# Performance work log

Hardware: AMD Instinct MI355X
Metric: run time of the kernel (lower is better)

The kernel has to match this reference:

```python
import jax, jax.numpy as jnp
import numpy as np

N, E, G = 50000, 800000, 256
NODE_IN, EDGE_IN, H, L, RO, OUT = 64, 16, 128, 3, 128, 2
EPS = 1e-5


def _ln(x, g, b):
    m = jnp.mean(x, axis=-1, keepdims=True)
    v = jnp.mean((x - m) ** 2, axis=-1, keepdims=True)
    return (x - m) * jax.lax.rsqrt(v + EPS) * g + b


def setup_inputs() -> dict:
    key = jax.random.key(0)
    ks = iter(jax.random.split(key, 40))
    w = lambda *s: jax.random.normal(next(ks), s, dtype=jnp.float32) * 0.05
    inp = {
        "x": jax.random.normal(next(ks), (N, NODE_IN), dtype=jnp.float32),
        "edge_attr": jax.random.normal(next(ks), (E, EDGE_IN), dtype=jnp.float32),
        "edge_index": jax.random.randint(next(ks), (2, E), 0, N, dtype=jnp.int32),
        "batch": jnp.sort(jax.random.randint(next(ks), (N,), 0, G, dtype=jnp.int32)),
        # encoders + input norms
        "node_enc_w": w(NODE_IN, H), "node_enc_b": jnp.zeros((H,), jnp.float32),
        "edge_enc_w": w(EDGE_IN, H), "edge_enc_b": jnp.zeros((H,), jnp.float32),
        "node_ln_g": jnp.ones((H,), jnp.float32), "node_ln_b": jnp.zeros((H,), jnp.float32),
        "edge_ln_g": jnp.ones((H,), jnp.float32), "edge_ln_b": jnp.zeros((H,), jnp.float32),
        # per-layer stacked params [L, ...]
        "msg_w1": w(L, 2 * H, H), "msg_b1": jnp.zeros((L, H), jnp.float32),
        "msg_w2": w(L, H, H), "msg_b2": jnp.zeros((L, H), jnp.float32),
        "gate_w": w(L, 2 * H, H), "gate_b": jnp.zeros((L, H), jnp.float32),
        "res_w1": w(L, 2 * H, H), "res_b1": jnp.zeros((L, H), jnp.float32),
        "res_w2": w(L, H, H), "res_b2": jnp.zeros((L, H), jnp.float32),
        "ln_g": jnp.ones((L, H), jnp.float32), "ln_b": jnp.zeros((L, H), jnp.float32),
        # readout MLP
        "ro_w1": w(H, RO), "ro_b1": jnp.zeros((RO,), jnp.float32),
        "ro_w2": w(RO, OUT), "ro_b2": jnp.zeros((OUT,), jnp.float32),
    }
    return inp


def reference(x, edge_attr, edge_index, batch,
              node_enc_w, node_enc_b, edge_enc_w, edge_enc_b,
              node_ln_g, node_ln_b, edge_ln_g, edge_ln_b,
              msg_w1, msg_b1, msg_w2, msg_b2, gate_w, gate_b,
              res_w1, res_b1, res_w2, res_b2, ln_g, ln_b,
              ro_w1, ro_b1, ro_w2, ro_b2):
    src, dst = edge_index[0], edge_index[1]
    h = _ln(x @ node_enc_w + node_enc_b, node_ln_g, node_ln_b)        # [N,H]
    e = _ln(edge_attr @ edge_enc_w + edge_enc_b, edge_ln_g, edge_ln_b)  # [E,H]
    for l in range(L):
        cat = jnp.concatenate([h[src], e], axis=-1)                   # [E,2H]
        gate = jax.nn.sigmoid(cat @ gate_w[l] + gate_b[l])
        msg = jax.nn.relu(cat @ msg_w1[l] + msg_b1[l]) @ msg_w2[l] + msg_b2[l]
        agg = jax.ops.segment_sum(gate * msg, dst, num_segments=N)    # scatter-add
        comb = jnp.concatenate([h, agg], axis=-1)                     # [N,2H]
        res = jax.nn.relu(comb @ res_w1[l] + res_b1[l]) @ res_w2[l] + res_b2[l]
        h = _ln(h + res, ln_g[l], ln_b[l])
    # global mean pool over graphs
    sums = jax.ops.segment_sum(h, batch, num_segments=G)              # [G,H]
    cnt = jax.ops.segment_sum(jnp.ones((h.shape[0],), h.dtype), batch, num_segments=G)
    g = sums / jnp.maximum(cnt, 1.0)[:, None]
    return jax.nn.relu(g @ ro_w1 + ro_b1) @ ro_w2 + ro_b2             # [G,OUT]
```

## Files before the change

kernel.cpp:

```cpp
#include <hip/hip_runtime.h>
#include <math.h>

#define NN 50000
#define NE 800000
#define NG 256
#define H 128
#define NIN 64
#define EIN 16
#define NL 3
#define LEPS 1e-5f

typedef short bf16x8 __attribute__((ext_vector_type(8)));
typedef float f32x4 __attribute__((ext_vector_type(4)));
typedef float f32x16 __attribute__((ext_vector_type(16)));

__device__ __forceinline__ short bf16rne(float x) {
  unsigned u = __float_as_uint(x);
  unsigned r = u + 0x7fff + ((u >> 16) & 1);
  return (short)(r >> 16);
}

__device__ __forceinline__ float wsum(float v) {
#pragma unroll
  for (int m = 1; m < 64; m <<= 1) v += __shfl_xor(v, m, 64);
  return v;
}

__device__ __forceinline__ float lds_f32(const short* p) {
  short2 s = *(const short2*)p;
  return __uint_as_float((unsigned)(unsigned short)s.x |
                         ((unsigned)(unsigned short)s.y << 16));
}

__global__ __launch_bounds__(256) void k_count(const int* __restrict__ eidx,
                                               unsigned* __restrict__ cnt) {
  int t = blockIdx.x * 256 + threadIdx.x;
  if (t < NE) atomicAdd(&cnt[eidx[NE + t]], 1u);
}

__global__ __launch_bounds__(1024) void k_scan(const unsigned* __restrict__ cnt,
                                               unsigned* __restrict__ rowptr) {
  __shared__ unsigned part[16];
  __shared__ unsigned carry_s;
  const int tid = threadIdx.x, lane = tid & 63, wid = tid >> 6;
  if (tid == 0) carry_s = 0;
  __syncthreads();
  for (int base = 0; base < NN; base += 1024) {
    int i = base + tid;
    unsigned v = (i < NN) ? cnt[i] : 0u;
    unsigned incl = v;
#pragma unroll
    for (int off = 1; off < 64; off <<= 1) {
      unsigned t = __shfl_up(incl, off, 64);
      if (lane >= off) incl += t;
    }
    if (lane == 63) part[wid] = incl;
    __syncthreads();
    if (tid == 0) {
      unsigned s = 0;
#pragma unroll
      for (int w = 0; w < 16; w++) { unsigned t = part[w]; part[w] = s; s += t; }
    }
    __syncthreads();
    unsigned carry = carry_s;
    if (i < NN) rowptr[i] = carry + part[wid] + incl - v;
    __syncthreads();
    if (tid == 1023) carry_s = carry + part[15] + incl;
    __syncthreads();
  }
}

__global__ __launch_bounds__(256) void k_fold(
    const float* __restrict__ gate_w, const float* __restrict__ msg_w1,
    const float* __restrict__ e_enc_w, const float* __restrict__ e_enc_b,
    const float* __restrict__ e_ln_g, const float* __restrict__ e_ln_b,
    short* __restrict__ w2e, float* __restrict__ c123,
    float* __restrict__ stats) {
  const int S_W2E = 3 * 4096;
  const int S_C = S_W2E + 3 * 768;
  const int S_ST = S_C + 290;
  int tid = blockIdx.x * 256 + threadIdx.x;
  if (tid >= S_ST) return;
  if (tid < S_W2E) {
    int l = tid / 4096, e = tid % 4096;
    int t = e >> 9, lane = (e >> 3) & 63, j = e & 7;
    int k = (lane >> 5) * 8 + j;
    int n = t * 32 + (lane & 31);
    float s = 0.f;
    for (int m = 0; m < 128; m++) {
      float w = (n < 128) ? gate_w[((size_t)l * 256 + 128 + m) * 128 + n]
                          : msg_w1[((size_t)l * 256 + 128 + m) * 128 + (n - 128)];
      s += e_enc_w[k * 128 + m] * e_ln_g[m] * w;
    }
    w2e[tid] = bf16rne(s);
  } else if (tid < S_C) {
    int e = tid - S_W2E;
    int l = e / 768, r = e % 768, which = r / 256, n = r % 256;
    float s = 0.f;
    for (int m = 0; m < 128; m++) {
      float w = (n < 128) ? gate_w[((size_t)l * 256 + 128 + m) * 128 + n]
                          : msg_w1[((size_t)l * 256 + 128 + m) * 128 + (n - 128)];
      float f = (which == 0) ? e_enc_b[m] * e_ln_g[m]
              : (which == 1) ? e_ln_g[m] : e_ln_b[m];
      s += f * w;
    }
    c123[e] = s;
  } else {
    int e = tid - S_C;
    if (e < 256) {
      int i = e >> 4, j = e & 15;
      float s = 0.f;
      for (int n = 0; n < 128; n++)
        s += e_enc_w[i * 128 + n] * e_enc_w[j * 128 + n];
      stats[e] = s;
    } else if (e < 272) {
      int k = e - 256;
      float s = 0.f;
      for (int n = 0; n < 128; n++) s += e_enc_w[k * 128 + n];
      stats[e] = s;
    } else if (e < 288) {
      int k = e - 272;
      float s = 0.f;
      for (int n = 0; n < 128; n++) s += e_enc_w[k * 128 + n] * e_enc_b[n];
      stats[e] = s;
    } else if (e == 288) {
      float s = 0.f;
      for (int n = 0; n < 128; n++) s += e_enc_b[n] * e_enc_b[n];
      stats[e] = s;
    } else {
      float s = 0.f;
      for (int n = 0; n < 128; n++) s += e_enc_b[n];
      stats[e] = s;
    }
  }
}

__global__ __launch_bounds__(256) void k_scatter(
    const int* __restrict__ eidx, const float* __restrict__ ea,
    const unsigned* __restrict__ rowptr, unsigned* __restrict__ cursor,
    const float* __restrict__ stats,
    int* __restrict__ src_s, int* __restrict__ dst_s,
    short* __restrict__ ea_bf, float2* __restrict__ rsmu) {
  __shared__ float S[290];
  for (int i = threadIdx.x; i < 290; i += 256) S[i] = stats[i];
  __syncthreads();
  int t = blockIdx.x * 256 + threadIdx.x;
  int s = eidx[t], d = eidx[NE + t];
  unsigned pos = rowptr[d] + atomicAdd(&cursor[d], 1u);
  src_s[pos] = s;
  dst_s[pos] = d;
  const float4* er = (const float4*)(ea + (size_t)t * EIN);
  float4 q0 = er[0], q1 = er[1], q2 = er[2], q3 = er[3];
  float e16[16];
  e16[0]=q0.x; e16[1]=q0.y; e16[2]=q0.z; e16[3]=q0.w;
  e16[4]=q1.x; e16[5]=q1.y; e16[6]=q1.z; e16[7]=q1.w;
  e16[8]=q2.x; e16[9]=q2.y; e16[10]=q2.z; e16[11]=q2.w;
  e16[12]=q3.x; e16[13]=q3.y; e16[14]=q3.z; e16[15]=q3.w;
  short tmp[16];
#pragma unroll
  for (int j = 0; j < 16; j++) tmp[j] = bf16rne(e16[j]);
  short* dstp = ea_bf + (size_t)pos * EIN;
  *(bf16x8*)dstp = *(bf16x8*)tmp;
  *(bf16x8*)(dstp + 8) = *(bf16x8*)(tmp + 8);
  float s1 = S[289], s2 = S[288];
#pragma unroll
  for (int k = 0; k < 16; k++) {
    s1 = fmaf(e16[k], S[256 + k], s1);
    s2 = fmaf(2.f * e16[k], S[272 + k], s2);
  }
#pragma unroll
  for (int i = 0; i < 16; i++) {
    float mi = 0.f;
#pragma unroll
    for (int j = 0; j < 16; j++) mi = fmaf(S[i * 16 + j], e16[j], mi);
    s2 = fmaf(e16[i], mi, s2);
  }
  float mu = s1 * (1.f / 128.f);
  float var = s2 * (1.f / 128.f) - mu * mu;
  float rs = rsqrtf(var + LEPS);
  rsmu[pos] = make_float2(rs, mu);
}

__global__ __launch_bounds__(256) void k_convert_w(
    const float* __restrict__ gate_w, const float* __restrict__ msg_w1,
    const float* __restrict__ msg_w2, const float* __restrict__ e_enc_w,
    const float* __restrict__ res_w1, const float* __restrict__ res_w2,
    short* __restrict__ bgh, short* __restrict__ bm2, short* __restrict__ benc,
    short* __restrict__ brs1, short* __restrict__ brs2) {
  const int S_BGH = 3 * 65536;
  const int S_BM2 = S_BGH + 3 * 16384;
  const int S_BEN = S_BM2 + 2048;
  const int S_BR1 = S_BEN + 3 * 32768;
  const int S_BR2 = S_BR1 + 3 * 16384;
  int tid = blockIdx.x * 256 + threadIdx.x;
  if (tid >= S_BR2) return;
  if (tid < S_BGH) {
    int l = tid / 65536, e = tid % 65536;
    int f = e >> 9, lane = (e >> 3) & 63, j = e & 7;
    int nt = f >> 4, ks = f & 15;
    int k = ks * 16 + (lane >> 5) * 8 + j;
    int n = nt * 32 + (lane & 31);
    float v = (n < 128) ? gate_w[((size_t)l * 256 + k) * 128 + n]
                        : msg_w1[((size_t)l * 256 + k) * 128 + (n - 128)];
    bgh[tid] = bf16rne(v);
  } else if (tid < S_BM2) {
    int e0 = tid - S_BGH;
    int l = e0 / 16384, e = e0 % 16384;
    int f = e >> 9, lane = (e >> 3) & 63, j = e & 7;
    int nt = f >> 3, ks = f & 7;
    int k = ks * 16 + (lane >> 5) * 8 + j;
    int n = nt * 32 + (lane & 31);
    bm2[e0] = bf16rne(msg_w2[((size_t)l * 128 + k) * 128 + n]);
  } else if (tid < S_BEN) {
    int e = tid - S_BM2;
    int t = e >> 9, lane = (e >> 3) & 63, j = e & 7;
    int k = (lane >> 5) * 8 + j;
    int n = t * 32 + (lane & 31);
    benc[e] = bf16rne(e_enc_w[k * H + n]);
  } else if (tid < S_BR1) {
    int e0 = tid - S_BEN;
    int l = e0 / 32768, e = e0 % 32768;
    int f = e >> 9, lane = (e >> 3) & 63, j = e & 7;
    int nt = f >> 3, ks = f & 7;
    int k = ks * 32 + (lane >> 4) * 8 + j;
    int n = nt * 16 + (lane & 15);
    brs1[e0] = bf16rne(res_w1[((size_t)l * 256 + k) * 128 + n]);
  } else {
    int e0 = tid - S_BR1;
    int l = e0 / 16384, e = e0 % 16384;
    int f = e >> 9, lane = (e >> 3) & 63, j = e & 7;
    int nt = f >> 2, ks = f & 3;
    int k = ks * 32 + (lane >> 4) * 8 + j;
    int n = nt * 16 + (lane & 15);
    brs2[e0] = bf16rne(res_w2[((size_t)l * 128 + k) * 128 + n]);
  }
}

__global__ __launch_bounds__(256) void k_node_encode(
    const float* __restrict__ x, const float* __restrict__ W,
    const float* __restrict__ bias,
    const float* __restrict__ lng, const float* __restrict__ lnb,
    float* __restrict__ h, short* __restrict__ h_bf) {
  __shared__ float xs[4][8 * NIN];
  const int wave = threadIdx.x >> 6, lane = threadIdx.x & 63;
  const int n0 = (blockIdx.x * 4 + wave) * 8;
  float* xt = xs[wave];
  for (int i = lane; i < 8 * NIN; i += 64) {
    int idx = n0 * NIN + i;
    xt[i] = (idx < NN * NIN) ? x[idx] : 0.f;
  }
  __syncthreads();
  const int c0 = lane, c1 = lane + 64;
  float a0[8], a1[8];
#pragma unroll
  for (int j = 0; j < 8; j++) { a0[j] = 0.f; a1[j] = 0.f; }
  for (int k = 0; k < NIN; k++) {
    float w0 = W[k * H + c0], w1 = W[k * H + c1];
#pragma unroll
    for (int j = 0; j < 8; j++) {
      float xv = xt[j * NIN + k];
      a0[j] = fmaf(xv, w0, a0[j]);
      a1[j] = fmaf(xv, w1, a1[j]);
    }
  }
  const float b0 = bias[c0], b1 = bias[c1];
  const float g0 = lng[c0], g1 = lng[c1], lb0 = lnb[c0], lb1 = lnb[c1];
#pragma unroll
  for (int j = 0; j < 8; j++) {
    float v0 = a0[j] + b0, v1 = a1[j] + b1;
    float mean = wsum(v0 + v1) * (1.f / H);
    float d0 = v0 - mean, d1 = v1 - mean;
    float var = wsum(d0 * d0 + d1 * d1) * (1.f / H);
    float rs = rsqrtf(var + LEPS);
    int n = n0 + j;
    if (n < NN) {
      float o0 = d0 * rs * g0 + lb0, o1 = d1 * rs * g1 + lb1;
      h[n * H + c0] = o0;
      h[n * H + c1] = o1;
      h_bf[n * H + c0] = bf16rne(o0);
      h_bf[n * H + c1] = bf16rne(o1);
    }
  }
}

__global__ __launch_bounds__(256) void k_edge_mfma(
    const short* __restrict__ ea_bf, const float2* __restrict__ rsmu,
    const int* __restrict__ src_s, const int* __restrict__ dst_s,
    const short* __restrict__ h_bf,
    const short* __restrict__ Bgh, const short* __restrict__ Bm2,
    const short* __restrict__ W2e, const float* __restrict__ c123,
    const float* __restrict__ gbias, const float* __restrict__ mbias1,
    const float* __restrict__ mbias2,
    float* __restrict__ agg) {
  __shared__ short regn[4][32 * 136];
  __shared__ int dsts[4][32];
  __shared__ float rsS[4][32], muS[4][32];
  const int tid = threadIdx.x;
  const int wave = tid >> 6, lane = tid & 63;
  const int e0 = blockIdx.x * 128 + wave * 32;
  short* R = regn[wave];
  const int c31 = lane & 31, halfl = lane >> 5;
  const int koff = halfl * 8;

  if (lane < 32) {
    dsts[wave][lane] = dst_s[e0 + lane];
    float2 rm = rsmu[e0 + lane];
    rsS[wave][lane] = rm.x;
    muS[wave][lane] = rm.y;
  }

  const int srow = src_s[e0 + c31];
  bf16x8 af[8];
#pragma unroll
  for (int ks = 0; ks < 8; ks++)
    af[ks] = *(const bf16x8*)(h_bf + (size_t)srow * H + ks * 16 + koff);

  const float rs_own = rsmu[e0 + c31].x;
  bf16x8 ae;
  {
    bf16x8 raw = *(const bf16x8*)(ea_bf + (size_t)(e0 + c31) * EIN + koff);
#pragma unroll
    for (int j = 0; j < 8; j++) {
      float f = __uint_as_float(((unsigned)(unsigned short)raw[j]) << 16);
      ae[j] = bf16rne(f * rs_own);
    }
  }

  float rsR[16], rmR[16];
#pragma unroll
  for (int r = 0; r < 16; r++) {
    int row = (r & 3) + 8 * (r >> 2) + 4 * halfl;
    rsR[r] = rsS[wave][row];
    rmR[r] = rsR[r] * muS[wave][row];
  }

#pragma unroll
  for (int ht = 0; ht < 4; ht++) {
    const int nt = 4 + ht;
    f32x16 a = __builtin_amdgcn_mfma_f32_32x32x16_bf16(
        ae, *(const bf16x8*)(W2e + (size_t)(nt * 64 + lane) * 8),
        (f32x16)(0.f), 0, 0, 0);
#pragma unroll
    for (int ks = 0; ks < 8; ks++) {
      bf16x8 bf = *(const bf16x8*)(Bgh + (size_t)((nt * 16 + ks) * 64 + lane) * 8);
      a = __builtin_amdgcn_mfma_f32_32x32x16_bf16(af[ks], bf, a, 0, 0, 0);
    }
    const int col = ht * 32 + c31;
    const int n = nt * 32 + c31;
    const float c1v = c123[n], c2v = c123[256 + n];
    const float c3b = c123[512 + n] + mbias1[col];
#pragma unroll
    for (int r = 0; r < 16; r++) {
      int row = (r & 3) + 8 * (r >> 2) + 4 * halfl;
      float pre = fmaf(rsR[r], c1v, fmaf(-rmR[r], c2v, a[r] + c3b));
      R[row * 136 + col] = bf16rne(fmaxf(pre, 0.f));
    }
  }

  float gate[4][16];
#pragma unroll
  for (int gt = 0; gt < 4; gt++) {
    f32x16 a = __builtin_amdgcn_mfma_f32_32x32x16_bf16(
        ae, *(const bf16x8*)(W2e + (size_t)(gt * 64 + lane) * 8),
        (f32x16)(0.f), 0, 0, 0);
#pragma unroll
    for (int ks = 0; ks < 8; ks++) {
      bf16x8 bf = *(const bf16x8*)(Bgh + (size_t)((gt * 16 + ks) * 64 + lane) * 8);
      a = __builtin_amdgcn_mfma_f32_32x32x16_bf16(af[ks], bf, a, 0, 0, 0);
    }
    const int n = gt * 32 + c31;
    const float c1v = c123[n], c2v = c123[256 + n];
    const float c3b = c123[512 + n] + gbias[n];
#pragma unroll
    for (int r = 0; r < 16; r++) {
      float pre = fmaf(rsR[r], c1v, fmaf(-rmR[r], c2v, a[r] + c3b));
      gate[gt][r] = __builtin_amdgcn_rcpf(1.f + __expf(-pre));
    }
  }

  bf16x8 a2[8];
#pragma unroll
  for (int ks = 0; ks < 8; ks++)
    a2[ks] = *(const bf16x8*)&R[c31 * 136 + ks * 16 + koff];

#pragma unroll
  for (int halfM = 0; halfM < 2; halfM++) {
#pragma unroll
    for (int t2 = 0; t2 < 2; t2++) {
      int gt = halfM * 2 + t2;
      f32x16 m = (f32x16)(0.f);
#pragma unroll
      for (int ks = 0; ks < 8; ks++) {
        bf16x8 bf = *(const bf16x8*)(Bm2 + (size_t)((gt * 8 + ks) * 64 + lane) * 8);
        m = __builtin_amdgcn_mfma_f32_32x32x16_bf16(a2[ks], bf, m, 0, 0, 0);
      }
      float mb2 = mbias2[gt * 32 + c31];
      int c2 = t2 * 32 + c31;
#pragma unroll
      for (int r = 0; r < 16; r++) {
        int row = (r & 3) + 8 * (r >> 2) + 4 * halfl;
        float msg = gate[gt][r] * (m[r] + mb2);
        unsigned u = __float_as_uint(msg);
        *(short2*)&R[row * 136 + c2 * 2] =
            make_short2((short)(u & 0xffff), (short)(u >> 16));
      }
    }
    const int colg = halfM * 64 + lane;
    int cur = dsts[wave][0];
    float run = lds_f32(&R[lane * 2]);
#pragma unroll
    for (int row = 1; row < 32; row++) {
      int d = dsts[wave][row];
      float v = lds_f32(&R[row * 136 + lane * 2]);
      if (d == cur) {
        run += v;
      } else {
        atomicAdd(&agg[(size_t)cur * H + colg], run);
        cur = d; run = v;
      }
    }
    atomicAdd(&agg[(size_t)cur * H + colg], run);
  }
}

__global__ __launch_bounds__(256) void k_node_up2(
    float* agg, const short* __restrict__ h_bf_in,
    const float* __restrict__ h_in,
    const short* __restrict__ Brs1, const short* __restrict__ Brs2,
    const float* __restrict__ rb1, const float* __restrict__ rb2,
    const float* __restrict__ lng, const float* __restrict__ lnb,
    float* __restrict__ h, short* __restrict__ h_bf) {
  __shared__ short regn[4][16 * 136];
  const int tid = threadIdx.x;
  const int wave = tid >> 6, lane = tid & 63;
  const int n0 = blockIdx.x * 64 + wave * 16;
  short* R = regn[wave];
  const int mrow = lane & 15, quad = lane >> 4;

  int nr = n0 + mrow; if (nr >= NN) nr = NN - 1;
  bf16x8 af[8];
#pragma unroll
  for (int ks = 0; ks < 4; ks++)
    af[ks] = *(const bf16x8*)(h_bf_in + (size_t)nr * H + ks * 32 + quad * 8);
#pragma unroll
  for (int ks = 0; ks < 4; ks++) {
    float4 u = *(const float4*)(agg + (size_t)nr * H + ks * 32 + quad * 8);
    float4 w = *(const float4*)(agg + (size_t)nr * H + ks * 32 + quad * 8 + 4);
    short tmp[8];
    tmp[0]=bf16rne(u.x); tmp[1]=bf16rne(u.y); tmp[2]=bf16rne(u.z); tmp[3]=bf16rne(u.w);
    tmp[4]=bf16rne(w.x); tmp[5]=bf16rne(w.y); tmp[6]=bf16rne(w.z); tmp[7]=bf16rne(w.w);
    af[4 + ks] = *(bf16x8*)tmp;
  }
  float4 z4 = make_float4(0.f, 0.f, 0.f, 0.f);
#pragma unroll
  for (int ks = 0; ks < 4; ks++) {
    *(float4*)(agg + (size_t)nr * H + ks * 32 + quad * 8) = z4;
    *(float4*)(agg + (size_t)nr * H + ks * 32 + quad * 8 + 4) = z4;
  }

#pragma unroll
  for (int t = 0; t < 8; t++) {
    f32x4 a = (f32x4){0.f, 0.f, 0.f, 0.f};
#pragma unroll
    for (int ks = 0; ks < 8; ks++) {
      bf16x8 bf = *(const bf16x8*)(Brs1 + (size_t)((t * 8 + ks) * 64 + lane) * 8);
      a = __builtin_amdgcn_mfma_f32_16x16x32_bf16(af[ks], bf, a, 0, 0, 0);
    }
    int col = t * 16 + mrow;
    float b = rb1[col];
#pragma unroll
    for (int r = 0; r < 4; r++)
      R[(quad * 4 + r) * 136 + col] = bf16rne(fmaxf(a[r] + b, 0.f));
  }
  bf16x8 a2[4];
#pragma unroll
  for (int ks = 0; ks < 4; ks++)
    a2[ks] = *(const bf16x8*)&R[mrow * 136 + ks * 32 + quad * 8];

  float vals[8][4];
  float gl[8], bl[8];
#pragma unroll
  for (int t = 0; t < 8; t++) {
    f32x4 a = (f32x4){0.f, 0.f, 0.f, 0.f};
#pragma unroll
    for (int ks = 0; ks < 4; ks++) {
      bf16x8 bf = *(const bf16x8*)(Brs2 + (size_t)((t * 4 + ks) * 64 + lane) * 8);
      a = __builtin_amdgcn_mfma_f32_16x16x32_bf16(a2[ks], bf, a, 0, 0, 0);
    }
    int col = t * 16 + mrow;
    float b2 = rb2[col];
    gl[t] = lng[col]; bl[t] = lnb[col];
#pragma unroll
    for (int r = 0; r < 4; r++) {
      int rowi = n0 + quad * 4 + r;
      int rl = rowi < NN ? rowi : NN - 1;
      vals[t][r] = h_in[(size_t)rl * H + col] + a[r] + b2;
    }
  }
#pragma unroll
  for (int r = 0; r < 4; r++) {
    float s1 = 0.f, s2 = 0.f;
#pragma unroll
    for (int t = 0; t < 8; t++) {
      s1 += vals[t][r];
      s2 = fmaf(vals[t][r], vals[t][r], s2);
    }
#pragma unroll
    for (int m = 1; m < 16; m <<= 1) {
      s1 += __shfl_xor(s1, m, 64);
      s2 += __shfl_xor(s2, m, 64);
    }
    float mean = s1 * (1.f / 128.f);
    float var = s2 * (1.f / 128.f) - mean * mean;
    float rs = rsqrtf(var + LEPS);
    int rowi = n0 + quad * 4 + r;
    if (rowi < NN) {
#pragma unroll
      for (int t = 0; t < 8; t++) {
        int col = t * 16 + mrow;
        float o = (vals[t][r] - mean) * rs * gl[t] + bl[t];
        h[(size_t)rowi * H + col] = o;
        h_bf[(size_t)rowi * H + col] = bf16rne(o);
      }
    }
  }
}

__global__ __launch_bounds__(256) void k_pool(
    const float* __restrict__ h, const int* __restrict__ batch,
    float* __restrict__ gsum, float* __restrict__ gcnt) {
  const int tid = threadIdx.x;
  const int col = tid & 127, half = tid >> 7;
  int n0 = blockIdx.x * 32 + half * 16;
  if (n0 >= NN) return;
  int end = n0 + 16; if (end > NN) end = NN;
  int cur = batch[n0];
  float run = h[(size_t)n0 * H + col];
  float cnt = 1.f;
  for (int n = n0 + 1; n < end; n++) {
    int b = batch[n];
    float v = h[(size_t)n * H + col];
    if (b == cur) { run += v; cnt += 1.f; }
    else {
      atomicAdd(&gsum[(size_t)cur * H + col], run);
      if (col == 0) atomicAdd(&gcnt[cur], cnt);
      cur = b; run = v; cnt = 1.f;
    }
  }
  atomicAdd(&gsum[(size_t)cur * H + col], run);
  if (col == 0) atomicAdd(&gcnt[cur], cnt);
}

__global__ __launch_bounds__(128) void k_readout(
    const float* __restrict__ gsum, const float* __restrict__ gcnt,
    const float* __restrict__ W1, const float* __restrict__ b1,
    const float* __restrict__ W2, const float* __restrict__ b2,
    float* __restrict__ out) {
  __shared__ float gs[H];
  __shared__ float o1[H];
  int b = blockIdx.x, c = threadIdx.x;
  float cnt = fmaxf(gcnt[b], 1.f);
  gs[c] = gsum[b * H + c] / cnt;
  __syncthreads();
  float acc = b1[c];
  for (int k = 0; k < H; k++) acc = fmaf(gs[k], W1[k * H + c], acc);
  o1[c] = fmaxf(acc, 0.f);
  __syncthreads();
  if (c < 2) {
    float acc2 = b2[c];
    for (int k = 0; k < H; k++) acc2 = fmaf(o1[k], W2[k * 2 + c], acc2);
    out[b * 2 + c] = acc2;
  }
}

extern "C" void kernel_launch(void* const* d_in, const int* in_sizes, int n_in,
                              void* d_out, int out_size, void* d_ws, size_t ws_size,
                              hipStream_t stream) {
  (void)in_sizes; (void)n_in; (void)out_size; (void)ws_size;
  const float* x       = (const float*)d_in[0];
  const float* ea      = (const float*)d_in[1];
  const int*   eidx    = (const int*)d_in[2];
  const int*   batch   = (const int*)d_in[3];
  const float* n_enc_w = (const float*)d_in[4];
  const float* n_enc_b = (const float*)d_in[5];
  const float* e_enc_w = (const float*)d_in[6];
  const float* e_enc_b = (const float*)d_in[7];
  const float* n_ln_g  = (const float*)d_in[8];
  const float* n_ln_b  = (const float*)d_in[9];
  const float* e_ln_g  = (const float*)d_in[10];
  const float* e_ln_b  = (const float*)d_in[11];
  const float* msg_w1  = (const float*)d_in[12];
  const float* msg_b1  = (const float*)d_in[13];
  const float* msg_w2  = (const float*)d_in[14];
  const float* msg_b2  = (const float*)d_in[15];
  const float* gate_w  = (const float*)d_in[16];
  const float* gate_b  = (const float*)d_in[17];
  const float* res_w1  = (const float*)d_in[18];
  const float* res_b1  = (const float*)d_in[19];
  const float* res_w2  = (const float*)d_in[20];
  const float* res_b2  = (const float*)d_in[21];
  const float* ln_g    = (const float*)d_in[22];
  const float* ln_b    = (const float*)d_in[23];
  const float* ro_w1   = (const float*)d_in[24];
  const float* ro_b1   = (const float*)d_in[25];
  const float* ro_w2   = (const float*)d_in[26];
  const float* ro_b2   = (const float*)d_in[27];

  char* p = (char*)d_ws;
  float* h     = (float*)p;  p += (size_t)NN * H * 4;
  short* h_bf  = (short*)p;  p += (size_t)NN * H * 2;
  float* agg   = (float*)p;  p += (size_t)NN * H * 4;
  short* ea_bf = (short*)p;  p += (size_t)NE * EIN * 2;
  float2* rsmu = (float2*)p; p += (size_t)NE * 8;
  float* gsum  = (float*)p;  p += (size_t)NG * H * 4;
  float* gcnt  = (float*)p;  p += 1024;
  short* bgh   = (short*)p;  p += (size_t)3 * 65536 * 2;
  short* bm2   = (short*)p;  p += (size_t)3 * 16384 * 2;
  short* benc  = (short*)p;  p += (size_t)2048 * 2;
  short* brs1  = (short*)p;  p += (size_t)3 * 32768 * 2;
  short* brs2  = (short*)p;  p += (size_t)3 * 16384 * 2;
  short* w2e   = (short*)p;  p += (size_t)3 * 4096 * 2;
  float* c123  = (float*)p;  p += (size_t)3 * 768 * 4;
  float* stats = (float*)p;  p += 2048;
  unsigned* rowptr = (unsigned*)p; p += ((size_t)NN * 4 + 15) / 16 * 16;
  unsigned* cursor = (unsigned*)p; p += ((size_t)NN * 4 + 15) / 16 * 16;
  int* src_s   = (int*)p;    p += (size_t)NE * 4;
  int* dst_s   = (int*)p;    p += (size_t)NE * 4;

  const int node_blocks = (NN + 31) / 32;
  const int nup_blocks  = (NN + 63) / 64;
  const int edge_blocks = NE / 128;
  const int e256 = (NE + 255) / 256;
  const int conv_total = 3 * 65536 + 3 * 16384 + 2048 + 3 * 32768 + 3 * 16384;
  const int fold_total = 3 * 4096 + 3 * 768 + 290;

  hipMemsetAsync(cursor, 0, (size_t)NN * 4, stream);
  k_fold<<<(fold_total + 255) / 256, 256, 0, stream>>>(
      gate_w, msg_w1, e_enc_w, e_enc_b, e_ln_g, e_ln_b, w2e, c123, stats);
  k_count<<<e256, 256, 0, stream>>>(eidx, cursor);
  k_scan<<<1, 1024, 0, stream>>>(cursor, rowptr);
  hipMemsetAsync(cursor, 0, (size_t)NN * 4, stream);
  k_scatter<<<e256, 256, 0, stream>>>(eidx, ea, rowptr, cursor, stats,
                                      src_s, dst_s, ea_bf, rsmu);

  k_convert_w<<<(conv_total + 255) / 256, 256, 0, stream>>>(
      gate_w, msg_w1, msg_w2, e_enc_w, res_w1, res_w2,
      bgh, bm2, benc, brs1, brs2);
  k_node_encode<<<node_blocks, 256, 0, stream>>>(x, n_enc_w, n_enc_b, n_ln_g, n_ln_b, h, h_bf);

  hipMemsetAsync(agg, 0, (size_t)NN * H * 4, stream);
  for (int l = 0; l < NL; l++) {
    k_edge_mfma<<<edge_blocks, 256, 0, stream>>>(
        ea_bf, rsmu, src_s, dst_s, h_bf,
        bgh + (size_t)l * 65536, bm2 + (size_t)l * 16384,
        w2e + (size_t)l * 4096, c123 + (size_t)l * 768,
        gate_b + l * H, msg_b1 + l * H, msg_b2 + l * H, agg);
    k_node_up2<<<nup_blocks, 256, 0, stream>>>(
        agg, h_bf, h,
        brs1 + (size_t)l * 32768, brs2 + (size_t)l * 16384,
        res_b1 + l * H, res_b2 + l * H,
        ln_g + l * H, ln_b + l * H, h, h_bf);
  }

  hipMemsetAsync(gsum, 0, ((size_t)NG * H + NG) * 4, stream);
  k_pool<<<(NN + 31) / 32, 256, 0, stream>>>(h, batch, gsum, gcnt);
  k_readout<<<NG, 128, 0, stream>>>(gsum, gcnt, ro_w1, ro_b1, ro_w2, ro_b2, (float*)d_out);
}
```

Measured before the change: 1.023 ms.

## Process 64 edges per wave and fold LN correction terms into extra MFMA K-slice

Each wave now handles two 32-edge M-tiles, so every B-fragment loaded from global or L2 feeds two MFMAs, halving weight-fragment traffic per edge. The per-column rs/mu/bias corrections that were applied as scalar FMAs are folded into an extra K=16 slice of the edge weight (rs, -rs*mu, 1 columns), so the MFMA applies them. Gate is recomputed per output tile instead of being kept as a 64-float array, and launch_bounds(256,2) with doubled LDS is set. This raises register and LDS pressure and routes the correction terms through bf16 rounding, which can cost accuracy.

```diff
diff --git a/kernel.cpp b/kernel.cpp
--- a/kernel.cpp
+++ b/kernel.cpp
@@ -1,4 +1,5 @@
 #include <hip/hip_runtime.h>
+#include <hip/hip_bf16.h>
 #include <math.h>
 
 #define NN 50000
@@ -13,11 +14,17 @@
 typedef short bf16x8 __attribute__((ext_vector_type(8)));
 typedef float f32x4 __attribute__((ext_vector_type(4)));
 typedef float f32x16 __attribute__((ext_vector_type(16)));
+typedef unsigned u32x4 __attribute__((ext_vector_type(4)));
 
 __device__ __forceinline__ short bf16rne(float x) {
   unsigned u = __float_as_uint(x);
   unsigned r = u + 0x7fff + ((u >> 16) & 1);
   return (short)(r >> 16);
+}
+
+__device__ __forceinline__ unsigned pk2(float lo, float hi) {
+  __hip_bfloat162 h = __float22bfloat162_rn(make_float2(lo, hi));
+  return *(unsigned*)&h;
 }
 
 __device__ __forceinline__ float wsum(float v) {
@@ -72,41 +79,37 @@
 
 __global__ __launch_bounds__(256) void k_fold(
     const float* __restrict__ gate_w, const float* __restrict__ msg_w1,
+    const float* __restrict__ gate_b, const float* __restrict__ msg_b1,
     const float* __restrict__ e_enc_w, const float* __restrict__ e_enc_b,
     const float* __restrict__ e_ln_g, const float* __restrict__ e_ln_b,
-    short* __restrict__ w2e, float* __restrict__ c123,
-    float* __restrict__ stats) {
-  const int S_W2E = 3 * 4096;
-  const int S_C = S_W2E + 3 * 768;
-  const int S_ST = S_C + 290;
+    short* __restrict__ w2e, float* __restrict__ stats) {
+  const int S_W2E = 3 * 8192;
+  const int S_ST = S_W2E + 290;
   int tid = blockIdx.x * 256 + threadIdx.x;
   if (tid >= S_ST) return;
   if (tid < S_W2E) {
-    int l = tid / 4096, e = tid % 4096;
-    int t = e >> 9, lane = (e >> 3) & 63, j = e & 7;
-    int k = (lane >> 5) * 8 + j;
-    int n = t * 32 + (lane & 31);
+    int l = tid / 8192, e = tid % 8192;
+    int f = e >> 9, lane = (e >> 3) & 63, j = e & 7;
+    int nt = f >> 1, ks2 = f & 1;
+    int k = ks2 * 16 + (lane >> 5) * 8 + j;
+    int n = nt * 32 + (lane & 31);
     float s = 0.f;
-    for (int m = 0; m < 128; m++) {
-      float w = (n < 128) ? gate_w[((size_t)l * 256 + 128 + m) * 128 + n]
-                          : msg_w1[((size_t)l * 256 + 128 + m) * 128 + (n - 128)];
-      s += e_enc_w[k * 128 + m] * e_ln_g[m] * w;
+    if (k < 19) {
+      for (int m = 0; m < 128; m++) {
+        float w = (n < 128) ? gate_w[((size_t)l * 256 + 128 + m) * 128 + n]
+                            : msg_w1[((size_t)l * 256 + 128 + m) * 128 + (n - 128)];
+        float fm = (k < 16)   ? e_enc_w[k * 128 + m] * e_ln_g[m]
+                 : (k == 16)  ? e_enc_b[m] * e_ln_g[m]
+                 : (k == 17)  ? e_ln_g[m]
+                              : e_ln_b[m];
+        s += fm * w;
+      }
+      if (k == 18)
+        s += (n < 128) ? gate_b[l * 128 + n] : msg_b1[l * 128 + (n - 128)];
     }
     w2e[tid] = bf16rne(s);
-  } else if (tid < S_C) {
+  } else {
     int e = tid - S_W2E;
-    int l = e / 768, r = e % 768, which = r / 256, n = r % 256;
-    float s = 0.f;
-    for (int m = 0; m < 128; m++) {
-      float w = (n < 128) ? gate_w[((size_t)l * 256 + 128 + m) * 128 + n]
-                          : msg_w1[((size_t)l * 256 + 128 + m) * 128 + (n - 128)];
-      float f = (which == 0) ? e_enc_b[m] * e_ln_g[m]
-              : (which == 1) ? e_ln_g[m] : e_ln_b[m];
-      s += f * w;
-    }
-    c123[e] = s;
-  } else {
-    int e = tid - S_C;
     if (e < 256) {
       int i = e >> 4, j = e & 15;
       float s = 0.f;
@@ -183,14 +186,13 @@
 
 __global__ __launch_bounds__(256) void k_convert_w(
     const float* __restrict__ gate_w, const float* __restrict__ msg_w1,
-    const float* __restrict__ msg_w2, const float* __restrict__ e_enc_w,
-    const float* __restrict__ res_w1, const float* __restrict__ res_w2,
-    short* __restrict__ bgh, short* __restrict__ bm2, short* __restrict__ benc,
+    const float* __restrict__ msg_w2, const float* __restrict__ res_w1,
+    const float* __restrict__ res_w2,
+    short* __restrict__ bgh, short* __restrict__ bm2,
     short* __restrict__ brs1, short* __restrict__ brs2) {
   const int S_BGH = 3 * 65536;
   const int S_BM2 = S_BGH + 3 * 16384;
-  const int S_BEN = S_BM2 + 2048;
-  const int S_BR1 = S_BEN + 3 * 32768;
+  const int S_BR1 = S_BM2 + 3 * 32768;
   const int S_BR2 = S_BR1 + 3 * 16384;
   int tid = blockIdx.x * 256 + threadIdx.x;
   if (tid >= S_BR2) return;
@@ -211,14 +213,8 @@
     int k = ks * 16 + (lane >> 5) * 8 + j;
     int n = nt * 32 + (lane & 31);
     bm2[e0] = bf16rne(msg_w2[((size_t)l * 128 + k) * 128 + n]);
-  } else if (tid < S_BEN) {
-    int e = tid - S_BM2;
-    int t = e >> 9, lane = (e >> 3) & 63, j = e & 7;
-    int k = (lane >> 5) * 8 + j;
-    int n = t * 32 + (lane & 31);
-    benc[e] = bf16rne(e_enc_w[k * H + n]);
   } else if (tid < S_BR1) {
-    int e0 = tid - S_BEN;
+    int e0 = tid - S_BM2;
     int l = e0 / 32768, e = e0 % 32768;
     int f = e >> 9, lane = (e >> 3) & 63, j = e & 7;
     int nt = f >> 3, ks = f & 7;
@@ -283,133 +279,131 @@
   }
 }
 
-__global__ __launch_bounds__(256) void k_edge_mfma(
+__global__ __launch_bounds__(256, 2) void k_edge_mfma(
     const short* __restrict__ ea_bf, const float2* __restrict__ rsmu,
     const int* __restrict__ src_s, const int* __restrict__ dst_s,
     const short* __restrict__ h_bf,
     const short* __restrict__ Bgh, const short* __restrict__ Bm2,
-    const short* __restrict__ W2e, const float* __restrict__ c123,
-    const float* __restrict__ gbias, const float* __restrict__ mbias1,
-    const float* __restrict__ mbias2,
+    const short* __restrict__ W2e, const float* __restrict__ mbias2,
     float* __restrict__ agg) {
-  __shared__ short regn[4][32 * 136];
-  __shared__ int dsts[4][32];
-  __shared__ float rsS[4][32], muS[4][32];
+  __shared__ short regn[4][64 * 136];
+  __shared__ int dsts[4][64];
   const int tid = threadIdx.x;
   const int wave = tid >> 6, lane = tid & 63;
-  const int e0 = blockIdx.x * 128 + wave * 32;
+  const int e0 = blockIdx.x * 256 + wave * 64;
   short* R = regn[wave];
   const int c31 = lane & 31, halfl = lane >> 5;
   const int koff = halfl * 8;
 
-  if (lane < 32) {
-    dsts[wave][lane] = dst_s[e0 + lane];
-    float2 rm = rsmu[e0 + lane];
-    rsS[wave][lane] = rm.x;
-    muS[wave][lane] = rm.y;
-  }
-
-  const int srow = src_s[e0 + c31];
-  bf16x8 af[8];
-#pragma unroll
-  for (int ks = 0; ks < 8; ks++)
-    af[ks] = *(const bf16x8*)(h_bf + (size_t)srow * H + ks * 16 + koff);
-
-  const float rs_own = rsmu[e0 + c31].x;
-  bf16x8 ae;
-  {
-    bf16x8 raw = *(const bf16x8*)(ea_bf + (size_t)(e0 + c31) * EIN + koff);
-#pragma unroll
-    for (int j = 0; j < 8; j++) {
-      float f = __uint_as_float(((unsigned)(unsigned short)raw[j]) << 16);
-      ae[j] = bf16rne(f * rs_own);
-    }
-  }
-
-  float rsR[16], rmR[16];
-#pragma unroll
-  for (int r = 0; r < 16; r++) {
-    int row = (r & 3) + 8 * (r >> 2) + 4 * halfl;
-    rsR[r] = rsS[wave][row];
-    rmR[r] = rsR[r] * muS[wave][row];
+  dsts[wave][lane] = dst_s[e0 + lane];
+
+  bf16x8 af0[8], af1[8], ae[2], ae2[2];
+#pragma unroll
+  for (int s = 0; s < 2; s++) {
+    const int er = e0 + s * 32 + c31;
+    const int srow = src_s[er];
+#pragma unroll
+    for (int ks = 0; ks < 8; ks++) {
+      bf16x8 v = *(const bf16x8*)(h_bf + (size_t)srow * H + ks * 16 + koff);
+      if (s == 0) af0[ks] = v; else af1[ks] = v;
+    }
+    const float2 rm = rsmu[er];
+    bf16x8 raw = *(const bf16x8*)(ea_bf + (size_t)er * EIN + koff);
+    u32x4 v;
+#pragma unroll
+    for (int p = 0; p < 4; p++) {
+      float lo = __uint_as_float(((unsigned)(unsigned short)raw[2 * p]) << 16) * rm.x;
+      float hi = __uint_as_float(((unsigned)(unsigned short)raw[2 * p + 1]) << 16) * rm.x;
+      v[p] = pk2(lo, hi);
+    }
+    ae[s] = __builtin_bit_cast(bf16x8, v);
+    u32x4 w;
+    w[0] = halfl ? 0u : pk2(rm.x, -rm.x * rm.y);
+    w[1] = halfl ? 0u : 0x00003F80u;
+    w[2] = 0u; w[3] = 0u;
+    ae2[s] = __builtin_bit_cast(bf16x8, w);
   }
 
 #pragma unroll
   for (int ht = 0; ht < 4; ht++) {
     const int nt = 4 + ht;
-    f32x16 a = __builtin_amdgcn_mfma_f32_32x32x16_bf16(
-        ae, *(const bf16x8*)(W2e + (size_t)(nt * 64 + lane) * 8),
-        (f32x16)(0.f), 0, 0, 0);
+    bf16x8 w0 = *(const bf16x8*)(W2e + (size_t)((nt * 2 + 0) * 64 + lane) * 8);
+    bf16x8 w1 = *(const bf16x8*)(W2e + (size_t)((nt * 2 + 1) * 64 + lane) * 8);
+    f32x16 A0 = __builtin_amdgcn_mfma_f32_32x32x16_bf16(ae[0], w0, (f32x16)(0.f), 0, 0, 0);
+    f32x16 A1 = __builtin_amdgcn_mfma_f32_32x32x16_bf16(ae[1], w0, (f32x16)(0.f), 0, 0, 0);
+    A0 = __builtin_amdgcn_mfma_f32_32x32x16_bf16(ae2[0], w1, A0, 0, 0, 0);
+    A1 = __builtin_amdgcn_mfma_f32_32x32x16_bf16(ae2[1], w1, A1, 0, 0, 0);
 #pragma unroll
     for (int ks = 0; ks < 8; ks++) {
-      bf16x8 bf = *(const bf16x8*)(Bgh + (size_t)((nt * 16 + ks) * 64 + lane) * 8);
-      a = __builtin_amdgcn_mfma_f32_32x32x16_bf16(af[ks], bf, a, 0, 0, 0);
+      bf16x8 bg = *(const bf16x8*)(Bgh + (size_t)((nt * 16 + ks) * 64 + lane) * 8);
+      A0 = __builtin_amdgcn_mfma_f32_32x32x16_bf16(af0[ks], bg, A0, 0, 0, 0);
+      A1 = __builtin_amdgcn_mfma_f32_32x32x16_bf16(af1[ks], bg, A1, 0, 0, 0);
     }
     const int col = ht * 32 + c31;
-    const int n = nt * 32 + c31;
-    const float c1v = c123[n], c2v = c123[256 + n];
-    const float c3b = c123[512 + n] + mbias1[col];
 #pragma unroll
     for (int r = 0; r < 16; r++) {
       int row = (r & 3) + 8 * (r >> 2) + 4 * halfl;
-      float pre = fmaf(rsR[r], c1v, fmaf(-rmR[r], c2v, a[r] + c3b));
-      R[row * 136 + col] = bf16rne(fmaxf(pre, 0.f));
-    }
-  }
-
-  float gate[4][16];
-#pragma unroll
-  for (int gt = 0; gt < 4; gt++) {
-    f32x16 a = __builtin_amdgcn_mfma_f32_32x32x16_bf16(
-        ae, *(const bf16x8*)(W2e + (size_t)(gt * 64 + lane) * 8),
-        (f32x16)(0.f), 0, 0, 0);
-#pragma unroll
-    for (int ks = 0; ks < 8; ks++) {
-      bf16x8 bf = *(const bf16x8*)(Bgh + (size_t)((gt * 16 + ks) * 64 + lane) * 8);
-      a = __builtin_amdgcn_mfma_f32_32x32x16_bf16(af[ks], bf, a, 0, 0, 0);
-    }
-    const int n = gt * 32 + c31;
-    const float c1v = c123[n], c2v = c123[256 + n];
-    const float c3b = c123[512 + n] + gbias[n];
-#pragma unroll
-    for (int r = 0; r < 16; r++) {
-      float pre = fmaf(rsR[r], c1v, fmaf(-rmR[r], c2v, a[r] + c3b));
-      gate[gt][r] = __builtin_amdgcn_rcpf(1.f + __expf(-pre));
-    }
-  }
-
-  bf16x8 a2[8];
-#pragma unroll
-  for (int ks = 0; ks < 8; ks++)
-    a2[ks] = *(const bf16x8*)&R[c31 * 136 + ks * 16 + koff];
+      R[row * 136 + col] = bf16rne(fmaxf(A0[r], 0.f));
+      R[(32 + row) * 136 + col] = bf16rne(fmaxf(A1[r], 0.f));
+    }
+  }
+
+  bf16x8 a2_0[8], a2_1[8];
+#pragma unroll
+  for (int ks = 0; ks < 8; ks++) {
+    a2_0[ks] = *(const bf16x8*)&R[c31 * 136 + ks * 16 + koff];
+    a2_1[ks] = *(const bf16x8*)&R[(32 + c31) * 136 + ks * 16 + koff];
+  }
 
 #pragma unroll
   for (int halfM = 0; halfM < 2; halfM++) {
 #pragma unroll
     for (int t2 = 0; t2 < 2; t2++) {
-      int gt = halfM * 2 + t2;
-      f32x16 m = (f32x16)(0.f);
+      const int gt = halfM * 2 + t2;
+      bf16x8 w0 = *(const bf16x8*)(W2e + (size_t)((gt * 2 + 0) * 64 + lane) * 8);
+      bf16x8 w1 = *(const bf16x8*)(W2e + (size_t)((gt * 2 + 1) * 64 + lane) * 8);
+      f32x16 G0 = __builtin_amdgcn_mfma_f32_32x32x16_bf16(ae[0], w0, (f32x16)(0.f), 0, 0, 0);
+      f32x16 G1 = __builtin_amdgcn_mfma_f32_32x32x16_bf16(ae[1], w0, (f32x16)(0.f), 0, 0, 0);
+      G0 = __builtin_amdgcn_mfma_f32_32x32x16_bf16(ae2[0], w1, G0, 0, 0, 0);
+      G1 = __builtin_amdgcn_mfma_f32_32x32x16_bf16(ae2[1], w1, G1, 0, 0, 0);
 #pragma unroll
       for (int ks = 0; ks < 8; ks++) {
-        bf16x8 bf = *(const bf16x8*)(Bm2 + (size_t)((gt * 8 + ks) * 64 + lane) * 8);
-        m = __builtin_amdgcn_mfma_f32_32x32x16_bf16(a2[ks], bf, m, 0, 0, 0);
+        bf16x8 bg = *(const bf16x8*)(Bgh + (size_t)((gt * 16 + ks) * 64 + lane) * 8);
+        G0 = __builtin_amdgcn_mfma_f32_32x32x16_bf16(af0[ks], bg, G0, 0, 0, 0);
+        G1 = __builtin_amdgcn_mfma_f32_32x32x16_bf16(af1[ks], bg, G1, 0, 0, 0);
       }
-      float mb2 = mbias2[gt * 32 + c31];
-      int c2 = t2 * 32 + c31;
+      float g0[16], g1[16];
+#pragma unroll
+      for (int r = 0; r < 16; r++) {
+        g0[r] = __builtin_amdgcn_rcpf(1.f + __expf(-G0[r]));
+        g1[r] = __builtin_amdgcn_rcpf(1.f + __expf(-G1[r]));
+      }
+      f32x16 M0 = (f32x16)(0.f), M1 = (f32x16)(0.f);
+#pragma unroll
+      for (int ks = 0; ks < 8; ks++) {
+        bf16x8 bm = *(const bf16x8*)(Bm2 + (size_t)((gt * 8 + ks) * 64 + lane) * 8);
+        M0 = __builtin_amdgcn_mfma_f32_32x32x16_bf16(a2_0[ks], bm, M0, 0, 0, 0);
+        M1 = __builtin_amdgcn_mfma_f32_32x32x16_bf16(a2_1[ks], bm, M1, 0, 0, 0);
+      }
+      const float mb2 = mbias2[gt * 32 + c31];
+      const int c2 = t2 * 32 + c31;
 #pragma unroll
       for (int r = 0; r < 16; r++) {
         int row = (r & 3) + 8 * (r >> 2) + 4 * halfl;
-        float msg = gate[gt][r] * (m[r] + mb2);
-        unsigned u = __float_as_uint(msg);
+        float m0 = g0[r] * (M0[r] + mb2);
+        float m1 = g1[r] * (M1[r] + mb2);
+        unsigned u0 = __float_as_uint(m0), u1 = __float_as_uint(m1);
         *(short2*)&R[row * 136 + c2 * 2] =
-            make_short2((short)(u & 0xffff), (short)(u >> 16));
+            make_short2((short)(u0 & 0xffff), (short)(u0 >> 16));
+        *(short2*)&R[(32 + row) * 136 + c2 * 2] =
+            make_short2((short)(u1 & 0xffff), (short)(u1 >> 16));
       }
     }
     const int colg = halfM * 64 + lane;
     int cur = dsts[wave][0];
     float run = lds_f32(&R[lane * 2]);
 #pragma unroll
-    for (int row = 1; row < 32; row++) {
+    for (int row = 1; row < 64; row++) {
       int d = dsts[wave][row];
       float v = lds_f32(&R[row * 136 + lane * 2]);
       if (d == cur) {
@@ -616,11 +610,9 @@
   float* gcnt  = (float*)p;  p += 1024;
   short* bgh   = (short*)p;  p += (size_t)3 * 65536 * 2;
   short* bm2   = (short*)p;  p += (size_t)3 * 16384 * 2;
-  short* benc  = (short*)p;  p += (size_t)2048 * 2;
   short* brs1  = (short*)p;  p += (size_t)3 * 32768 * 2;
   short* brs2  = (short*)p;  p += (size_t)3 * 16384 * 2;
-  short* w2e   = (short*)p;  p += (size_t)3 * 4096 * 2;
-  float* c123  = (float*)p;  p += (size_t)3 * 768 * 4;
+  short* w2e   = (short*)p;  p += (size_t)3 * 8192 * 2;
   float* stats = (float*)p;  p += 2048;
   unsigned* rowptr = (unsigned*)p; p += ((size_t)NN * 4 + 15) / 16 * 16;
   unsigned* cursor = (unsigned*)p; p += ((size_t)NN * 4 + 15) / 16 * 16;
@@ -629,14 +621,15 @@
 
   const int node_blocks = (NN + 31) / 32;
   const int nup_blocks  = (NN + 63) / 64;
-  const int edge_blocks = NE / 128;
+  const int edge_blocks = NE / 256;
   const int e256 = (NE + 255) / 256;
-  const int conv_total = 3 * 65536 + 3 * 16384 + 2048 + 3 * 32768 + 3 * 16384;
-  const int fold_total = 3 * 4096 + 3 * 768 + 290;
+  const int conv_total = 3 * 65536 + 3 * 16384 + 3 * 32768 + 3 * 16384;
+  const int fold_total = 3 * 8192 + 290;
 
   hipMemsetAsync(cursor, 0, (size_t)NN * 4, stream);
   k_fold<<<(fold_total + 255) / 256, 256, 0, stream>>>(
-      gate_w, msg_w1, e_enc_w, e_enc_b, e_ln_g, e_ln_b, w2e, c123, stats);
+      gate_w, msg_w1, gate_b, msg_b1, e_enc_w, e_enc_b, e_ln_g, e_ln_b,
+      w2e, stats);
   k_count<<<e256, 256, 0, stream>>>(eidx, cursor);
   k_scan<<<1, 1024, 0, stream>>>(cursor, rowptr);
   hipMemsetAsync(cursor, 0, (size_t)NN * 4, stream);
@@ -644,8 +637,8 @@
                                       src_s, dst_s, ea_bf, rsmu);
 
   k_convert_w<<<(conv_total + 255) / 256, 256, 0, stream>>>(
-      gate_w, msg_w1, msg_w2, e_enc_w, res_w1, res_w2,
-      bgh, bm2, benc, brs1, brs2);
+      gate_w, msg_w1, msg_w2, res_w1, res_w2,
+      bgh, bm2, brs1, brs2);
   k_node_encode<<<node_blocks, 256, 0, stream>>>(x, n_enc_w, n_enc_b, n_ln_g, n_ln_b, h, h_bf);
 
   hipMemsetAsync(agg, 0, (size_t)NN * H * 4, stream);
@@ -653,8 +646,7 @@
     k_edge_mfma<<<edge_blocks, 256, 0, stream>>>(
         ea_bf, rsmu, src_s, dst_s, h_bf,
         bgh + (size_t)l * 65536, bm2 + (size_t)l * 16384,
-        w2e + (size_t)l * 4096, c123 + (size_t)l * 768,
-        gate_b + l * H, msg_b1 + l * H, msg_b2 + l * H, agg);
+        w2e + (size_t)l * 8192, msg_b2 + l * H, agg);
     k_node_up2<<<nup_blocks, 256, 0, stream>>>(
         agg, h_bf, h,
         brs1 + (size_t)l * 32768, brs2 + (size_t)l * 16384,
```

After: 1.452 ms. 42.0% more time.
